# Optimization experiments

Measured on AMD Instinct MI355X. Metric: run time of the kernel, lower is better.

The kernel has to match this reference:

```python
import jax, jax.numpy as jnp
import numpy as np

N_ENT = 50000   # entities (nodes)
N_REL = 500     # relations
DEG = 32        # regular in-degree of the full KG
TOPK = 10       # topk in-edges kept per node by dgl.sampling.select_topk
H_DIM = 256
N_HEADS = 4
HEAD_DIM = H_DIM // N_HEADS
NEG_SLOPE = 0.2


def _leaky(x):
    return jnp.where(x >= 0, x, NEG_SLOPE * x)


def setup_inputs() -> dict:
    key = jax.random.key(0)
    ks = jax.random.split(key, 8)
    s = 0.05
    return {
        'ent_emb': jax.random.normal(ks[0], (N_ENT, H_DIM), dtype=jnp.float32),
        'rel_emb': jax.random.normal(ks[1], (N_REL, H_DIM), dtype=jnp.float32),
        'W': jax.random.normal(ks[2], (N_HEADS, H_DIM, HEAD_DIM), dtype=jnp.float32) * s,
        'W_r': jax.random.normal(ks[3], (N_HEADS, H_DIM, HEAD_DIM), dtype=jnp.float32) * s,
        'a': jax.random.normal(ks[4], (N_HEADS, 3 * HEAD_DIM), dtype=jnp.float32) * s,
        'neigh_w': jax.random.normal(ks[5], (H_DIM, H_DIM), dtype=jnp.float32) * s,
        'src': jax.random.randint(ks[6], (N_ENT, DEG), 0, N_ENT),   # src node of each in-edge of node n
        'rel_id': jax.random.randint(ks[7], (N_ENT, DEG), 0, N_REL),
    }


def reference(ent_emb, rel_emb, W, W_r, a, neigh_w, src, rel_id):
    # ---- head-0 scores used for top-k in-edge sampling (select_topk, edge_dir='in') ----
    emb_t0 = ent_emb @ W[0]          # [N, hd]
    rel_t0 = rel_emb @ W_r[0]        # [R, hd]
    a0 = a[0]
    # concat([src,dst,rel]) @ a  ==  src@a_src + dst@a_dst + rel@a_rel
    s_src = emb_t0 @ a0[:HEAD_DIM]                 # [N]
    s_dst = emb_t0 @ a0[HEAD_DIM:2 * HEAD_DIM]     # [N]
    s_rel = rel_t0 @ a0[2 * HEAD_DIM:]             # [R]
    score0 = _leaky(s_src[src] + s_dst[:, None] + s_rel[rel_id])   # [N, DEG]
    _, top_idx = jax.lax.top_k(score0, TOPK)                        # [N, K]
    src_sel = jnp.take_along_axis(src, top_idx, axis=1)             # [N, K]
    rel_sel = jnp.take_along_axis(rel_id, top_idx, axis=1)          # [N, K]

    # ---- all heads on the sampled subgraph (vectorized over heads) ----
    emb_t = jnp.einsum('nd,hde->hne', ent_emb, W)     # [H, N, hd]
    rel_t = jnp.einsum('rd,hde->hre', rel_emb, W_r)   # [H, R, hd]
    a3 = a.reshape(N_HEADS, 3, HEAD_DIM)
    ss = jnp.einsum('hne,he->hn', emb_t, a3[:, 0])    # [H, N]
    sd = jnp.einsum('hne,he->hn', emb_t, a3[:, 1])    # [H, N]
    sr = jnp.einsum('hre,he->hr', rel_t, a3[:, 2])    # [H, R]
    scores = _leaky(ss[:, src_sel] + sd[:, :, None] + sr[:, rel_sel])  # [H, N, K]
    norm = jax.nn.softmax(scores, axis=-1)            # edge-softmax over in-edges per dst

    # comp_op == 'add' : u_add_e, weighted by attention, summed into dst
    comp = emb_t[:, src_sel] + rel_t[:, rel_sel]      # [H, N, K, hd]
    neigh = jnp.einsum('hnke,hnk->hne', comp, norm)   # [H, N, hd]

    neigh = jnp.transpose(neigh, (1, 0, 2)).reshape(ent_emb.shape[0], H_DIM)  # concat heads
    return jnp.tanh(neigh @ neigh_w)                  # bn disabled (cfg.bn=False)
```

## Files before the change

kernel.cpp:

```cpp
#include <hip/hip_runtime.h>
#include <math.h>

#define N_ENT 50000
#define N_REL 500
#define DEG 32
#define TOPK 10
#define H_DIM 256
#define N_HEADS 4
#define HEAD_DIM 64

typedef __attribute__((ext_vector_type(8))) short short8v;
typedef __attribute__((ext_vector_type(4))) float f32x4;

constexpr size_t OFF_SSRC0 = 0;
constexpr size_t OFF_SR0   = 400000;
constexpr size_t OFF_U0    = 404000;
constexpr size_t OFF_V0    = 406048;
constexpr size_t OFF_SS    = 408096;
constexpr size_t OFF_SSR   = 2008096;
constexpr size_t OFF_U8    = 2024096;
constexpr size_t OFF_V8    = 2032288;
constexpr size_t OFF_B1H   = 2040480;
constexpr size_t OFF_B2H   = 2302624;
constexpr size_t OFF_B3H   = 2564768;
constexpr size_t OFF_RPK   = 2826912;
constexpr size_t OFF_EAH   = 3089056;
constexpr size_t OFF_EMBBF = 28713632;
constexpr size_t OFF_RELBF = 54313632;
constexpr size_t WS_NEED   = 54569632;

__device__ __forceinline__ float leaky(float x) { return x >= 0.f ? x : 0.2f * x; }

__device__ __forceinline__ unsigned short bf16_rne(float x) {
    unsigned int u = __float_as_uint(x);
    unsigned int r = u + 0x7fffu + ((u >> 16) & 1u);
    return (unsigned short)(r >> 16);
}
__device__ __forceinline__ float bf2f(unsigned short x) {
    return __uint_as_float((unsigned)x << 16);
}

__device__ __forceinline__ size_t pack_off(int row, int d) {
    return ((size_t)(row >> 4) * 8 + (d >> 5)) * 512 +
           (((d >> 3) & 3) * 16 + (row & 15)) * 8 + (d & 7);
}

__global__ __launch_bounds__(256) void setup_kernel(
    const float* __restrict__ W, const float* __restrict__ W_r,
    const float* __restrict__ a, const float* __restrict__ nw,
    float* __restrict__ U8, double* __restrict__ u0,
    float* __restrict__ V8, double* __restrict__ v0,
    unsigned short* __restrict__ b1h, unsigned short* __restrict__ b2h,
    unsigned short* __restrict__ b3h)
{
    const int bid = blockIdx.x;
    const int tid = threadIdx.x;
    if (bid == 0) {
        int d = tid;
        #pragma unroll
        for (int h = 0; h < N_HEADS; ++h) {
            float ss = 0.f, sd = 0.f;
            #pragma unroll
            for (int e = 0; e < HEAD_DIM; ++e) {
                float w = W[h * 16384 + d * 64 + e];
                ss += w * a[h * 192 + e];
                sd += w * a[h * 192 + 64 + e];
            }
            U8[d * 8 + h] = ss;
            U8[d * 8 + 4 + h] = sd;
        }
        double s0 = 0.0;
        #pragma unroll
        for (int e = 0; e < HEAD_DIM; ++e)
            s0 += (double)W[d * 64 + e] * (double)a[e];
        u0[d] = s0;
    } else if (bid == 1) {
        int d = tid;
        #pragma unroll
        for (int h = 0; h < N_HEADS; ++h) {
            float sv = 0.f;
            #pragma unroll
            for (int e = 0; e < HEAD_DIM; ++e)
                sv += W_r[h * 16384 + d * 64 + e] * a[h * 192 + 128 + e];
            V8[d * 8 + h] = sv;
            V8[d * 8 + 4 + h] = 0.f;
        }
        double s0 = 0.0;
        #pragma unroll
        for (int e = 0; e < HEAD_DIM; ++e)
            s0 += (double)W_r[d * 64 + e] * (double)a[128 + e];
        v0[d] = s0;
    } else {
        int n = bid - 2;
        int k = tid;
        int h = n >> 6, e = n & 63;
        float x1 = W[h * 16384 + k * 64 + e];
        float x2 = nw[k * 256 + n];
        float x3 = W_r[h * 16384 + k * 64 + e];
        size_t off = pack_off(n, k);
        b1h[off] = bf16_rne(x1);
        b2h[off] = bf16_rne(x2);
        b3h[off] = bf16_rne(x3);
    }
}

__global__ __launch_bounds__(256) void ss_kernel(
    const float* __restrict__ ent, const float* __restrict__ relm,
    const float* __restrict__ U8, const double* __restrict__ u0,
    const float* __restrict__ V8, const double* __restrict__ v0,
    float* __restrict__ SS, double* __restrict__ ssrc0, unsigned short* __restrict__ apk,
    float* __restrict__ SSR, double* __restrict__ sr0, unsigned short* __restrict__ rpk)
{
    const int tid = threadIdx.x;
    const int l = tid & 63;
    const int el = l & 31;
    const int q2 = l >> 5;

    const bool isent = blockIdx.x < 2048;
    const float* X = isent ? ent : relm;
    const float* U8v = isent ? U8 : V8;
    const double* u0v = isent ? u0 : v0;
    float* SSout = isent ? SS : SSR;
    double* s0out = isent ? ssrc0 : sr0;
    unsigned short* Xpk = isent ? apk : rpk;
    const int N = isent ? N_ENT : N_REL;
    const int wave = isent ? ((blockIdx.x * 256 + tid) >> 6)
                           : (((blockIdx.x - 2048) * 256 + tid) >> 6);
    const int nwaves = isent ? 8192 : 252;

    float uu[8][8];
    #pragma unroll
    for (int i = 0; i < 8; ++i) {
        float4 a4 = *(const float4*)(U8v + (el * 8 + i) * 8);
        float4 b4 = *(const float4*)(U8v + (el * 8 + i) * 8 + 4);
        uu[i][0] = a4.x; uu[i][1] = a4.y; uu[i][2] = a4.z; uu[i][3] = a4.w;
        uu[i][4] = b4.x; uu[i][5] = b4.y; uu[i][6] = b4.z; uu[i][7] = b4.w;
    }
    double ud[8];
    #pragma unroll
    for (int i = 0; i < 8; ++i) ud[i] = u0v[el * 8 + i];

    const int jout = ((el & 1) << 2) | (el & 2) | ((el >> 2) & 1);

    for (int p = wave; p < N / 2; p += nwaves) {
        int n = p * 2 + q2;
        float4 x1 = *(const float4*)(X + (size_t)n * 256 + el * 8);
        float4 x2 = *(const float4*)(X + (size_t)n * 256 + el * 8 + 4);
        float xs[8] = {x1.x, x1.y, x1.z, x1.w, x2.x, x2.y, x2.z, x2.w};

        short8v ov;
        #pragma unroll
        for (int i = 0; i < 8; ++i) ov[i] = (short)bf16_rne(xs[i]);
        *(short8v*)(Xpk + pack_off(n, el * 8)) = ov;

        float pj[8] = {0.f, 0.f, 0.f, 0.f, 0.f, 0.f, 0.f, 0.f};
        double pd = 0.0;
        #pragma unroll
        for (int i = 0; i < 8; ++i) {
            #pragma unroll
            for (int j = 0; j < 8; ++j) pj[j] += xs[i] * uu[i][j];
            pd += (double)xs[i] * ud[i];
        }

        const bool b1 = (el & 1);
        float q[4];
        #pragma unroll
        for (int j = 0; j < 4; ++j) {
            float mine = b1 ? pj[j + 4] : pj[j];
            float send = b1 ? pj[j] : pj[j + 4];
            q[j] = mine + __shfl_xor(send, 1);
        }
        const bool b2 = (el & 2);
        float r2[2];
        #pragma unroll
        for (int j = 0; j < 2; ++j) {
            float mine = b2 ? q[j + 2] : q[j];
            float send = b2 ? q[j] : q[j + 2];
            r2[j] = mine + __shfl_xor(send, 2);
        }
        const bool b4 = (el & 4);
        {
            float mine = b4 ? r2[1] : r2[0];
            float send = b4 ? r2[0] : r2[1];
            r2[0] = mine + __shfl_xor(send, 4);
        }
        r2[0] += __shfl_xor(r2[0], 8);
        r2[0] += __shfl_xor(r2[0], 16);

        #pragma unroll
        for (int off = 1; off < 32; off <<= 1) pd += __shfl_xor(pd, off);

        if (el < 8) SSout[(size_t)n * 8 + jout] = r2[0];
        if (el == 0) s0out[n] = pd;
    }
}

__global__ __launch_bounds__(256, 4) void gemm_hi(
    const unsigned short* __restrict__ A1, const unsigned short* __restrict__ B1,
    unsigned short* __restrict__ C1, int M1, int nb1,
    const unsigned short* __restrict__ A2, const unsigned short* __restrict__ B2,
    unsigned short* __restrict__ C2, int M2)
{
    const int tid = threadIdx.x;
    const int l = tid & 63;
    const int w = tid >> 6;
    const int rl = l & 15;
    const int ql = l >> 4;

    const int b = blockIdx.x;
    const unsigned short* Apk = (b < nb1) ? A1 : A2;
    const unsigned short* Bh  = (b < nb1) ? B1 : B2;
    unsigned short* C         = (b < nb1) ? C1 : C2;
    const int M               = (b < nb1) ? M1 : M2;
    const int bm              = ((b < nb1) ? b : (b - nb1)) * 64;

    const unsigned short* ab = Apk + (size_t)(bm >> 4) * 4096 + l * 8;
    const unsigned short* bhb = Bh + (size_t)w * 16384 + l * 8;

    f32x4 acc[4][4];
    #pragma unroll
    for (int i = 0; i < 4; ++i)
        #pragma unroll
        for (int j = 0; j < 4; ++j) acc[i][j] = (f32x4){0.f, 0.f, 0.f, 0.f};

    #pragma unroll
    for (int ks = 0; ks < 8; ++ks) {
        short8v ah[4], bh[4];
        #pragma unroll
        for (int mf = 0; mf < 4; ++mf)
            ah[mf] = *(const short8v*)(ab + mf * 4096 + ks * 512);
        #pragma unroll
        for (int nf = 0; nf < 4; ++nf)
            bh[nf] = *(const short8v*)(bhb + nf * 4096 + ks * 512);
        #pragma unroll
        for (int mf = 0; mf < 4; ++mf)
            #pragma unroll
            for (int nf = 0; nf < 4; ++nf)
                acc[mf][nf] = __builtin_amdgcn_mfma_f32_16x16x32_bf16(ah[mf], bh[nf], acc[mf][nf], 0, 0, 0);
    }

    #pragma unroll
    for (int mf = 0; mf < 4; ++mf) {
        int row0 = bm + mf * 16 + ql * 4;
        #pragma unroll
        for (int nf = 0; nf < 4; ++nf) {
            int c = w * 64 + nf * 16 + rl;
            #pragma unroll
            for (int j = 0; j < 4; ++j) {
                int r = row0 + j;
                if (r < M)
                    C[(size_t)r * 256 + c] = bf16_rne(acc[mf][nf][j]);
            }
        }
    }
}

__global__ __launch_bounds__(256, 3) void node_kernel(
    const int* __restrict__ src, const int* __restrict__ relid,
    const float* __restrict__ SS, const double* __restrict__ ssrc0,
    const float* __restrict__ SSR, const double* __restrict__ sr0,
    const unsigned short* __restrict__ emb_bf, const unsigned short* __restrict__ rel_bf,
    unsigned short* __restrict__ napk)
{
    __shared__ __align__(16) float sr4s[N_REL * 4];
    __shared__ double sr0s[N_REL];
    __shared__ float wls[8][32][4];

    const int tid = threadIdx.x;
    for (int i = tid; i < N_REL; i += 256) {
        *(float4*)&sr4s[i * 4] = *(const float4*)&SSR[i * 8];
        sr0s[i] = sr0[i];
    }
    __syncthreads();

    const int l = tid & 63;
    const int el = l & 31;
    const int hb = l & 32;
    const int nib = tid >> 5;
    const int n = blockIdx.x * 8 + nib;

    const int sd_ = src[n * DEG + el];
    const int rd_ = relid[n * DEG + el];
    const double sc0 = ssrc0[sd_] + sr0s[rd_];

    int cnt = 0;
    #pragma unroll
    for (int j = 0; j < DEG; ++j) {
        double sj = __shfl(sc0, hb | j);
        cnt += (sj > sc0 || (sj == sc0 && j < el)) ? 1 : 0;
    }
    const bool sel = (cnt < TOPK);
    const unsigned mask = (unsigned)(__ballot(sel) >> hb);

    float scx = -1e30f, scy = -1e30f, scz = -1e30f, scw = -1e30f;
    if (sel) {
        float4 ssv = *(const float4*)(SS + (size_t)sd_ * 8);
        float4 srv = *(const float4*)&sr4s[rd_ * 4];
        float4 sdv = *(const float4*)(SS + (size_t)n * 8 + 4);
        scx = leaky(ssv.x + sdv.x + srv.x);
        scy = leaky(ssv.y + sdv.y + srv.y);
        scz = leaky(ssv.z + sdv.z + srv.z);
        scw = leaky(ssv.w + sdv.w + srv.w);
    }

    float mx = scx, my = scy, mz = scz, mw = scw;
    #pragma unroll
    for (int off = 1; off < 32; off <<= 1) {
        mx = fmaxf(mx, __shfl_xor(mx, off));
        my = fmaxf(my, __shfl_xor(my, off));
        mz = fmaxf(mz, __shfl_xor(mz, off));
        mw = fmaxf(mw, __shfl_xor(mw, off));
    }
    float ex = sel ? __expf(scx - mx) : 0.f;
    float ey = sel ? __expf(scy - my) : 0.f;
    float ez = sel ? __expf(scz - mz) : 0.f;
    float ew = sel ? __expf(scw - mw) : 0.f;
    float sx = ex, sy = ey, sz = ez, sw = ew;
    #pragma unroll
    for (int off = 1; off < 32; off <<= 1) {
        sx += __shfl_xor(sx, off);
        sy += __shfl_xor(sy, off);
        sz += __shfl_xor(sz, off);
        sw += __shfl_xor(sw, off);
    }

    if (sel) {
        float4 wv; wv.x = ex; wv.y = ey; wv.z = ez; wv.w = ew;
        *(float4*)&wls[nib][el][0] = wv;
    }
    __syncthreads();

    const int h = el >> 3;
    const float sh = h == 0 ? sx : h == 1 ? sy : h == 2 ? sz : sw;
    const float rsh = 1.f / sh;

    int lks[TOPK], sk[TOPK], rk[TOPK];
    unsigned mm = mask;
    #pragma unroll
    for (int k = 0; k < TOPK; ++k) {
        lks[k] = __builtin_ctz(mm);
        mm &= mm - 1;
        sk[k] = __shfl(sd_, hb | lks[k]);
        rk[k] = __shfl(rd_, hb | lks[k]);
    }

    short8v ev[TOPK];
    #pragma unroll
    for (int k = 0; k < TOPK; ++k)
        ev[k] = *(const short8v*)(emb_bf + (size_t)sk[k] * 256 + el * 8);

    float acc[8] = {0.f, 0.f, 0.f, 0.f, 0.f, 0.f, 0.f, 0.f};
    #pragma unroll
    for (int k = 0; k < TOPK; ++k) {
        short8v rv = *(const short8v*)(rel_bf + (size_t)rk[k] * 256 + el * 8);
        float w = wls[nib][lks[k]][h] * rsh;
        #pragma unroll
        for (int j = 0; j < 8; ++j)
            acc[j] += w * (bf2f((unsigned short)ev[k][j]) + bf2f((unsigned short)rv[j]));
    }

    short8v ov;
    #pragma unroll
    for (int j = 0; j < 8; ++j) ov[j] = (short)bf16_rne(acc[j]);
    *(short8v*)(napk + pack_off(n, el * 8)) = ov;
}

__global__ __launch_bounds__(256, 4) void gemm_out(
    const unsigned short* __restrict__ Apk, const unsigned short* __restrict__ Bpkh,
    float* __restrict__ Cout, int M)
{
    const int tid = threadIdx.x;
    const int l = tid & 63;
    const int w = tid >> 6;
    const int bm = blockIdx.x * 64;
    const int rl = l & 15;
    const int ql = l >> 4;

    const unsigned short* ab = Apk + (size_t)(bm >> 4) * 4096 + l * 8;
    const unsigned short* bhb = Bpkh + (size_t)w * 16384 + l * 8;

    f32x4 acc[4][4];
    #pragma unroll
    for (int i = 0; i < 4; ++i)
        #pragma unroll
        for (int j = 0; j < 4; ++j) acc[i][j] = (f32x4){0.f, 0.f, 0.f, 0.f};

    #pragma unroll
    for (int ks = 0; ks < 8; ++ks) {
        short8v ah[4], bh[4];
        #pragma unroll
        for (int mf = 0; mf < 4; ++mf)
            ah[mf] = *(const short8v*)(ab + mf * 4096 + ks * 512);
        #pragma unroll
        for (int nf = 0; nf < 4; ++nf)
            bh[nf] = *(const short8v*)(bhb + nf * 4096 + ks * 512);
        #pragma unroll
        for (int mf = 0; mf < 4; ++mf)
            #pragma unroll
            for (int nf = 0; nf < 4; ++nf)
                acc[mf][nf] = __builtin_amdgcn_mfma_f32_16x16x32_bf16(ah[mf], bh[nf], acc[mf][nf], 0, 0, 0);
    }

    #pragma unroll
    for (int mf = 0; mf < 4; ++mf) {
        int row0 = bm + mf * 16 + ql * 4;
        #pragma unroll
        for (int nf = 0; nf < 4; ++nf) {
            int c = w * 64 + nf * 16 + rl;
            #pragma unroll
            for (int j = 0; j < 4; ++j) {
                int r = row0 + j;
                if (r < M) {
                    float v = acc[mf][nf][j];
                    Cout[(size_t)r * 256 + c] = 1.f - 2.f / (__expf(2.f * v) + 1.f);
                }
            }
        }
    }
}

extern "C" void kernel_launch(void* const* d_in, const int* in_sizes, int n_in,
                              void* d_out, int out_size, void* d_ws, size_t ws_size,
                              hipStream_t stream) {
    const float* ent  = (const float*)d_in[0];
    const float* rel  = (const float*)d_in[1];
    const float* W    = (const float*)d_in[2];
    const float* W_r  = (const float*)d_in[3];
    const float* a    = (const float*)d_in[4];
    const float* nw   = (const float*)d_in[5];
    const int*   srcp = (const int*)d_in[6];
    const int*   ridp = (const int*)d_in[7];
    float* out = (float*)d_out;

    if (ws_size < WS_NEED) return;

    char* ws = (char*)d_ws;
    double* ssrc0 = (double*)(ws + OFF_SSRC0);
    double* sr0   = (double*)(ws + OFF_SR0);
    double* u0    = (double*)(ws + OFF_U0);
    double* v0    = (double*)(ws + OFF_V0);
    float*  SS    = (float*)(ws + OFF_SS);
    float*  SSR   = (float*)(ws + OFF_SSR);
    float*  U8    = (float*)(ws + OFF_U8);
    float*  V8    = (float*)(ws + OFF_V8);
    unsigned short* b1h = (unsigned short*)(ws + OFF_B1H);
    unsigned short* b2h = (unsigned short*)(ws + OFF_B2H);
    unsigned short* b3h = (unsigned short*)(ws + OFF_B3H);
    unsigned short* rpk = (unsigned short*)(ws + OFF_RPK);
    unsigned short* apk = (unsigned short*)(ws + OFF_EAH);
    unsigned short* embbf = (unsigned short*)(ws + OFF_EMBBF);
    unsigned short* relbf = (unsigned short*)(ws + OFF_RELBF);
    unsigned short* napk = apk;

    setup_kernel<<<258, 256, 0, stream>>>(W, W_r, a, nw, U8, u0, V8, v0,
                                          b1h, b2h, b3h);
    ss_kernel<<<2111, 256, 0, stream>>>(ent, rel, U8, u0, V8, v0,
                                        SS, ssrc0, apk, SSR, sr0, rpk);
    gemm_hi<<<790, 256, 0, stream>>>(apk, b1h, embbf, N_ENT, 782,
                                     rpk, b3h, relbf, N_REL);
    node_kernel<<<6250, 256, 0, stream>>>(srcp, ridp, SS, ssrc0, SSR, sr0,
                                          embbf, relbf, napk);
    gemm_out<<<782, 256, 0, stream>>>(napk, b2h, out, N_ENT);
}
```

Before: 155.4 us.

## Prefetch projection rows and batch gather loads, dropping LDS staging in node kernel

The projection kernel now software-pipelines its row loads, fetching the next row's float4 pair before processing the current one. In node_kernel, the per-block copy of relation scores into shared memory is removed and the scores are read directly from global memory, which also removes both __syncthreads. The relation-embedding gathers are issued together with the entity gathers before the accumulate loop, behind an explicit vmcnt wait, to raise memory-level parallelism. The costs are higher register pressure and uncached global reads of the relation scores, which could lower occupancy.

```diff
diff --git a/kernel.cpp b/kernel.cpp
--- a/kernel.cpp
+++ b/kernel.cpp
@@ -124,8 +124,8 @@
     double* s0out = isent ? ssrc0 : sr0;
     unsigned short* Xpk = isent ? apk : rpk;
     const int N = isent ? N_ENT : N_REL;
-    const int wave = isent ? ((blockIdx.x * 256 + tid) >> 6)
-                           : (((blockIdx.x - 2048) * 256 + tid) >> 6);
+    const int wave0 = isent ? ((blockIdx.x * 256 + tid) >> 6)
+                            : (((blockIdx.x - 2048) * 256 + tid) >> 6);
     const int nwaves = isent ? 8192 : 252;
 
     float uu[8][8];
@@ -141,12 +141,25 @@
     for (int i = 0; i < 8; ++i) ud[i] = u0v[el * 8 + i];
 
     const int jout = ((el & 1) << 2) | (el & 2) | ((el >> 2) & 1);
-
-    for (int p = wave; p < N / 2; p += nwaves) {
-        int n = p * 2 + q2;
-        float4 x1 = *(const float4*)(X + (size_t)n * 256 + el * 8);
-        float4 x2 = *(const float4*)(X + (size_t)n * 256 + el * 8 + 4);
-        float xs[8] = {x1.x, x1.y, x1.z, x1.w, x2.x, x2.y, x2.z, x2.w};
+    const int half = N / 2;
+
+    int p = wave0;
+    float4 x1, x2;
+    if (p < half) {
+        int n0 = p * 2 + q2;
+        x1 = *(const float4*)(X + (size_t)n0 * 256 + el * 8);
+        x2 = *(const float4*)(X + (size_t)n0 * 256 + el * 8 + 4);
+    }
+    for (; p < half; p += nwaves) {
+        const int n = p * 2 + q2;
+        const float4 cx1 = x1, cx2 = x2;
+        const int np = p + nwaves;
+        if (np < half) {
+            int n1 = np * 2 + q2;
+            x1 = *(const float4*)(X + (size_t)n1 * 256 + el * 8);
+            x2 = *(const float4*)(X + (size_t)n1 * 256 + el * 8 + 4);
+        }
+        float xs[8] = {cx1.x, cx1.y, cx1.z, cx1.w, cx2.x, cx2.y, cx2.z, cx2.w};
 
         short8v ov;
         #pragma unroll
@@ -262,17 +275,9 @@
     const unsigned short* __restrict__ emb_bf, const unsigned short* __restrict__ rel_bf,
     unsigned short* __restrict__ napk)
 {
-    __shared__ __align__(16) float sr4s[N_REL * 4];
-    __shared__ double sr0s[N_REL];
     __shared__ float wls[8][32][4];
 
     const int tid = threadIdx.x;
-    for (int i = tid; i < N_REL; i += 256) {
-        *(float4*)&sr4s[i * 4] = *(const float4*)&SSR[i * 8];
-        sr0s[i] = sr0[i];
-    }
-    __syncthreads();
-
     const int l = tid & 63;
     const int el = l & 31;
     const int hb = l & 32;
@@ -281,7 +286,7 @@
 
     const int sd_ = src[n * DEG + el];
     const int rd_ = relid[n * DEG + el];
-    const double sc0 = ssrc0[sd_] + sr0s[rd_];
+    const double sc0 = ssrc0[sd_] + sr0[rd_];
 
     int cnt = 0;
     #pragma unroll
@@ -295,7 +300,7 @@
     float scx = -1e30f, scy = -1e30f, scz = -1e30f, scw = -1e30f;
     if (sel) {
         float4 ssv = *(const float4*)(SS + (size_t)sd_ * 8);
-        float4 srv = *(const float4*)&sr4s[rd_ * 4];
+        float4 srv = *(const float4*)(SSR + (size_t)rd_ * 8);
         float4 sdv = *(const float4*)(SS + (size_t)n * 8 + 4);
         scx = leaky(ssv.x + sdv.x + srv.x);
         scy = leaky(ssv.y + sdv.y + srv.y);
@@ -328,7 +333,6 @@
         float4 wv; wv.x = ex; wv.y = ey; wv.z = ez; wv.w = ew;
         *(float4*)&wls[nib][el][0] = wv;
     }
-    __syncthreads();
 
     const int h = el >> 3;
     const float sh = h == 0 ? sx : h == 1 ? sy : h == 2 ? sz : sw;
@@ -344,19 +348,22 @@
         rk[k] = __shfl(rd_, hb | lks[k]);
     }
 
-    short8v ev[TOPK];
+    short8v ev[TOPK], rv[TOPK];
     #pragma unroll
     for (int k = 0; k < TOPK; ++k)
         ev[k] = *(const short8v*)(emb_bf + (size_t)sk[k] * 256 + el * 8);
+    #pragma unroll
+    for (int k = 0; k < TOPK; ++k)
+        rv[k] = *(const short8v*)(rel_bf + (size_t)rk[k] * 256 + el * 8);
+    asm volatile("s_waitcnt vmcnt(0)" ::: "memory");
 
     float acc[8] = {0.f, 0.f, 0.f, 0.f, 0.f, 0.f, 0.f, 0.f};
     #pragma unroll
     for (int k = 0; k < TOPK; ++k) {
-        short8v rv = *(const short8v*)(rel_bf + (size_t)rk[k] * 256 + el * 8);
         float w = wls[nib][lks[k]][h] * rsh;
         #pragma unroll
         for (int j = 0; j < 8; ++j)
-            acc[j] += w * (bf2f((unsigned short)ev[k][j]) + bf2f((unsigned short)rv[j]));
+            acc[j] += w * (bf2f((unsigned short)ev[k][j]) + bf2f((unsigned short)rv[k][j]));
     }
 
     short8v ov;
```

Measured after the change: 146.9 us. 1.06x faster.
